# Kernel optimization log

Hardware: AMD Instinct MI355X
Metric: run time of the kernel (lower is better)

## Reference

```python
import jax, jax.numpy as jnp
import numpy as np

B, S, D, H = 2, 2048, 1024, 16
HD = D // H  # head_size = 64

def setup_inputs() -> dict:
    key = jax.random.key(0)
    ks = jax.random.split(key, 8)
    sc = 0.02
    return {
        "q": jax.random.normal(ks[0], (B, S, D), jnp.float32),
        "k": jax.random.normal(ks[1], (B, S, D), jnp.float32),
        "v": jax.random.normal(ks[2], (B, S, D), jnp.float32),
        "padding_mask": jnp.zeros((B, 1, 1, S), jnp.float32),
        "Wq": jax.random.normal(ks[3], (D, D), jnp.float32) * sc,
        "bq": jnp.zeros((D,), jnp.float32),
        "Wk": jax.random.normal(ks[4], (D, D), jnp.float32) * sc,
        "bk": jnp.zeros((D,), jnp.float32),
        "Wv": jax.random.normal(ks[5], (D, D), jnp.float32) * sc,
        "bv": jnp.zeros((D,), jnp.float32),
        "Wo": jax.random.normal(ks[6], (D, D), jnp.float32) * sc,
        "bo": jnp.zeros((D,), jnp.float32),
    }

def reference(q, k, v, padding_mask, Wq, bq, Wk, bk, Wv, bv, Wo, bo):
    b = q.shape[0]
    qh = (q @ Wq + bq).reshape(b, -1, H, HD)
    kh = (k @ Wk + bk).reshape(b, -1, H, HD)
    vh = (v @ Wv + bv).reshape(b, -1, H, HD)
    # [B, H, Sq, Sk] scores, materialized as in the original
    qk = jnp.einsum('bjhd,bkhd->bhjk', qh, kh) / jnp.sqrt(jnp.float32(HD))
    qk = qk + padding_mask * -1e12
    attn = jax.nn.softmax(qk, axis=-1)
    qkv = jnp.einsum('bhjk,bkhd->bjhd', attn, vh).reshape(b, -1, D)
    return qkv @ Wo + bo
```

## Files before the change

### kernel.cpp

```cpp
#include <hip/hip_runtime.h>
#include <math.h>

typedef __bf16 bf16_t;
typedef __bf16 bf16x8 __attribute__((ext_vector_type(8)));
typedef __bf16 bf16x4v __attribute__((ext_vector_type(4)));
typedef float f32x4 __attribute__((ext_vector_type(4)));
typedef float f32x16 __attribute__((ext_vector_type(16)));

#define LOG2E 1.4426950408889634f
#define MBIAS_C (-1e12f * LOG2E)

#if __has_builtin(__builtin_amdgcn_exp2f)
#define EXP2F(x) __builtin_amdgcn_exp2f(x)
#else
#define EXP2F(x) exp2f(x)
#endif

typedef __attribute__((address_space(1))) const unsigned int g_u32;
typedef __attribute__((address_space(3))) unsigned int l_u32;
__device__ __forceinline__ void load_lds_16B(const void* g, void* l){
  __builtin_amdgcn_global_load_lds((g_u32*)g, (l_u32*)l, 16, 0, 0);
}

__device__ __forceinline__ f32x16 zero16(){
  f32x16 z;
  #pragma unroll
  for (int i = 0; i < 16; i++) z[i] = 0.f;
  return z;
}

typedef union { bf16x4v b4; uint2 u2; } pk8;
typedef union { uint2 h[2]; bf16x8 b8; } pk16;
typedef union { float4 f4[4]; f32x16 v; } cinit_t;

__global__ __launch_bounds__(256) void cast3_kernel(const float* __restrict__ q,
                                                    const float* __restrict__ k,
                                                    const float* __restrict__ v,
                                                    bf16_t* __restrict__ out){
  int z = blockIdx.y;
  const float* x = (z == 0) ? q : (z == 1) ? k : v;
  int i = blockIdx.x * 256 + threadIdx.x;
  float4 f = reinterpret_cast<const float4*>(x)[i];
  bf16x4v w;
  w[0] = (bf16_t)f.x; w[1] = (bf16_t)f.y; w[2] = (bf16_t)f.z; w[3] = (bf16_t)f.w;
  reinterpret_cast<bf16x4v*>(out + (size_t)z * 4194304)[i] = w;
}

__global__ __launch_bounds__(256) void wtrans4_kernel(const float* __restrict__ Wq,
                                                      const float* __restrict__ Wk,
                                                      const float* __restrict__ Wv,
                                                      const float* __restrict__ Wo,
                                                      bf16_t* __restrict__ Wcat,
                                                      bf16_t* __restrict__ Wot){
  __shared__ float T[32][33];
  int z = blockIdx.z;
  const float* W = (z == 0) ? Wq : (z == 1) ? Wk : (z == 2) ? Wv : Wo;
  bf16_t* dst = (z < 3) ? (Wcat + (size_t)z * 1024 * 1024) : Wot;
  int x = threadIdx.x, y = threadIdx.y;
  int k0 = blockIdx.y * 32, n0 = blockIdx.x * 32;
  #pragma unroll
  for (int i = 0; i < 4; i++) T[y + 8*i][x] = W[(size_t)(k0 + y + 8*i) * 1024 + n0 + x];
  __syncthreads();
  #pragma unroll
  for (int i = 0; i < 4; i++) dst[(size_t)(n0 + y + 8*i) * 1024 + k0 + x] = (bf16_t)T[x][y + 8*i];
}

__device__ __forceinline__ void qkv_epilogue(f32x4 (&acc)[4][4], int seg, int n0g, int m0,
                                             int wm, int wn, int l16, int lq,
                                             const float* bias, bf16_t* qp, bf16_t* kp,
                                             bf16_t* vh){
  bf16_t* Cp = (seg == 0) ? qp : (seg == 1) ? kp : vh;
  float scale = (seg == 0) ? 0.125f * LOG2E : 1.0f;
  #pragma unroll
  for (int ti = 0; ti < 4; ti++){
    #pragma unroll
    for (int tj = 0; tj < 4; tj++){
      int col = (n0g + wn + tj*16 + l16) & 1023;
      float bvv = bias[col];
      #pragma unroll
      for (int r = 0; r < 4; r++){
        int row = m0 + wm + ti*16 + lq*4 + r;
        Cp[(size_t)row * 1024 + col] = (bf16_t)((acc[ti][tj][r] + bvv) * scale);
      }
    }
  }
}

__global__ __launch_bounds__(256) void gemm_qkv_bf(const bf16_t* __restrict__ qkvin,
                                                   const bf16_t* __restrict__ Wcat,
                                                   const float* __restrict__ bq,
                                                   const float* __restrict__ bk,
                                                   const float* __restrict__ bv,
                                                   bf16_t* __restrict__ qp,
                                                   bf16_t* __restrict__ kp,
                                                   bf16_t* __restrict__ vh){
  const int K = 1024;
  __shared__ __align__(16) bf16_t As[128*64];
  __shared__ __align__(16) bf16_t Bs[128*64];
  int tid = threadIdx.x, wave = tid >> 6, lane = tid & 63;
  int l16 = lane & 15, lq = lane >> 4;
  int m0  = blockIdx.x * 128;
  int n0g = blockIdx.y * 128;
  int seg = n0g >> 10;
  const bf16_t* A   = qkvin + (size_t)seg * 4194304;
  const float* bias = (seg == 0) ? bq : (seg == 1) ? bk : bv;
  int wm = (wave >> 1) * 64, wn = (wave & 1) * 64;
  f32x4 acc[4][4] = {};
  for (int kt = 0; kt < K; kt += 64){
    __syncthreads();
    #pragma unroll
    for (int i = 0; i < 4; i++){
      int u = tid + 256*i;
      int r = u >> 3, cpos = u & 7, cg = cpos ^ (r & 7);
      int ldsoff = (wave*64 + 256*i) * 16;
      load_lds_16B(&A[(size_t)(m0 + r) * K + kt + cg*8], (char*)As + ldsoff);
      load_lds_16B(&Wcat[(size_t)(n0g + r) * K + kt + cg*8], (char*)Bs + ldsoff);
    }
    __syncthreads();
    #pragma unroll
    for (int kk = 0; kk < 2; kk++){
      bf16x8 af[4], bfr[4];
      #pragma unroll
      for (int t = 0; t < 4; t++){
        int row = wm + t*16 + l16, cpos = (kk*4 + lq) ^ (l16 & 7);
        af[t] = *reinterpret_cast<bf16x8*>(&As[row*64 + cpos*8]);
      }
      #pragma unroll
      for (int t = 0; t < 4; t++){
        int row = wn + t*16 + l16, cpos = (kk*4 + lq) ^ (l16 & 7);
        bfr[t] = *reinterpret_cast<bf16x8*>(&Bs[row*64 + cpos*8]);
      }
      #pragma unroll
      for (int ti = 0; ti < 4; ti++)
        #pragma unroll
        for (int tj = 0; tj < 4; tj++)
          acc[ti][tj] = __builtin_amdgcn_mfma_f32_16x16x32_bf16(af[ti], bfr[tj], acc[ti][tj], 0, 0, 0);
    }
  }
  qkv_epilogue(acc, seg, n0g, m0, wm, wn, l16, lq, bias, qp, kp, vh);
}

__global__ __launch_bounds__(256) void gemm_qkv_f32(const float* __restrict__ qi,
                                                    const float* __restrict__ ki,
                                                    const float* __restrict__ vi,
                                                    const bf16_t* __restrict__ Wcat,
                                                    const float* __restrict__ bq,
                                                    const float* __restrict__ bk,
                                                    const float* __restrict__ bv,
                                                    bf16_t* __restrict__ qp,
                                                    bf16_t* __restrict__ kp,
                                                    bf16_t* __restrict__ vh){
  const int K = 1024;
  __shared__ __align__(16) float  Asf[128*32];
  __shared__ __align__(16) bf16_t Bs[128*32];
  int tid = threadIdx.x, wave = tid >> 6, lane = tid & 63;
  int l16 = lane & 15, lq = lane >> 4;
  int n0g = blockIdx.x * 128;
  int seg = n0g >> 10;
  const float* A    = (seg == 0) ? qi : (seg == 1) ? ki : vi;
  const float* bias = (seg == 0) ? bq : (seg == 1) ? bk : bv;
  int m0 = blockIdx.y * 128;
  int wm = (wave >> 1) * 64, wn = (wave & 1) * 64;
  int cposR = lq ^ ((l16 >> 2) & 3);
  int ca0 = (2*lq)     ^ (l16 & 7);
  int ca1 = (2*lq + 1) ^ (l16 & 7);
  f32x4 acc[4][4] = {};
  for (int kt = 0; kt < K; kt += 32){
    __syncthreads();
    #pragma unroll
    for (int i = 0; i < 4; i++){
      int u = tid + 256*i;
      int r = u >> 3, cpos = u & 7, cg = cpos ^ (r & 7);
      load_lds_16B(&A[(size_t)(m0 + r) * K + kt + cg*4], (char*)Asf + (wave*64 + 256*i)*16);
    }
    #pragma unroll
    for (int i = 0; i < 2; i++){
      int u = tid + 256*i;
      int r = u >> 2, cpos = u & 3, cg = cpos ^ ((r >> 2) & 3);
      load_lds_16B(&Wcat[(size_t)(n0g + r) * K + kt + cg*8], (char*)Bs + (wave*64 + 256*i)*16);
    }
    __syncthreads();
    bf16x8 af[4], bfr[4];
    #pragma unroll
    for (int t = 0; t < 4; t++){
      int row = wm + t*16 + l16;
      f32x4 x0 = *reinterpret_cast<f32x4*>(&Asf[row*32 + ca0*4]);
      f32x4 x1 = *reinterpret_cast<f32x4*>(&Asf[row*32 + ca1*4]);
      bf16x8 a;
      a[0] = (bf16_t)x0[0]; a[1] = (bf16_t)x0[1]; a[2] = (bf16_t)x0[2]; a[3] = (bf16_t)x0[3];
      a[4] = (bf16_t)x1[0]; a[5] = (bf16_t)x1[1]; a[6] = (bf16_t)x1[2]; a[7] = (bf16_t)x1[3];
      af[t] = a;
    }
    #pragma unroll
    for (int t = 0; t < 4; t++) bfr[t] = *reinterpret_cast<bf16x8*>(&Bs[(wn + t*16 + l16)*32 + cposR*8]);
    #pragma unroll
    for (int ti = 0; ti < 4; ti++)
      #pragma unroll
      for (int tj = 0; tj < 4; tj++)
        acc[ti][tj] = __builtin_amdgcn_mfma_f32_16x16x32_bf16(af[ti], bfr[tj], acc[ti][tj], 0, 0, 0);
  }
  qkv_epilogue(acc, seg, n0g, m0, wm, wn, l16, lq, bias, qp, kp, vh);
}

__global__ __launch_bounds__(256) void gemm_out(const bf16_t* __restrict__ A,
                                                const bf16_t* __restrict__ Bt,
                                                const float* __restrict__ bias,
                                                float* __restrict__ C){
  const int K = 1024, N = 1024;
  __shared__ __align__(16) bf16_t As[128*64];
  __shared__ __align__(16) bf16_t Bs[64*64];
  int tid = threadIdx.x, wave = tid >> 6, lane = tid & 63;
  int l16 = lane & 15, lq = lane >> 4;
  int m0 = blockIdx.x * 128, n0 = blockIdx.y * 64;
  int wm = wave * 32;
  f32x4 acc[2][4] = {};
  for (int kt = 0; kt < K; kt += 64){
    __syncthreads();
    #pragma unroll
    for (int i = 0; i < 4; i++){
      int u = tid + 256*i;
      int r = u >> 3, cpos = u & 7, cg = cpos ^ (r & 7);
      load_lds_16B(&A[(size_t)(m0 + r) * K + kt + cg*8], (char*)As + (wave*64 + 256*i)*16);
    }
    #pragma unroll
    for (int i = 0; i < 2; i++){
      int u = tid + 256*i;
      int r = u >> 3, cpos = u & 7, cg = cpos ^ (r & 7);
      load_lds_16B(&Bt[(size_t)(n0 + r) * K + kt + cg*8], (char*)Bs + (wave*64 + 256*i)*16);
    }
    __syncthreads();
    #pragma unroll
    for (int kk = 0; kk < 2; kk++){
      bf16x8 af[2], bfr[4];
      #pragma unroll
      for (int t = 0; t < 2; t++){
        int row = wm + t*16 + l16, cpos = (kk*4 + lq) ^ (l16 & 7);
        af[t] = *reinterpret_cast<bf16x8*>(&As[row*64 + cpos*8]);
      }
      #pragma unroll
      for (int t = 0; t < 4; t++){
        int row = t*16 + l16, cpos = (kk*4 + lq) ^ (l16 & 7);
        bfr[t] = *reinterpret_cast<bf16x8*>(&Bs[row*64 + cpos*8]);
      }
      #pragma unroll
      for (int ti = 0; ti < 2; ti++)
        #pragma unroll
        for (int tj = 0; tj < 4; tj++)
          acc[ti][tj] = __builtin_amdgcn_mfma_f32_16x16x32_bf16(af[ti], bfr[tj], acc[ti][tj], 0, 0, 0);
    }
  }
  #pragma unroll
  for (int ti = 0; ti < 2; ti++){
    #pragma unroll
    for (int tj = 0; tj < 4; tj++){
      int col = n0 + tj*16 + l16;
      float bvv = bias[col];
      #pragma unroll
      for (int r = 0; r < 4; r++){
        int row = m0 + wm + ti*16 + lq*4 + r;
        C[(size_t)row * N + col] = acc[ti][tj][r] + bvv;
      }
    }
  }
}

__global__ __launch_bounds__(256) void vtrans_kernel(const bf16_t* __restrict__ vh,
                                                     bf16_t* __restrict__ Vt){
  __shared__ bf16_t T[64][72];
  int tid = threadIdx.x;
  int s0 = blockIdx.x * 64, h = blockIdx.y, b = blockIdx.z;
  #pragma unroll
  for (int i = 0; i < 2; i++){
    int u = tid + 256*i;
    int r = u >> 3, c = (u & 7) * 8;
    *reinterpret_cast<uint4*>(&T[r][c]) =
      *reinterpret_cast<const uint4*>(&vh[(size_t)(b*2048 + s0 + r) * 1024 + h*64 + c]);
  }
  __syncthreads();
  #pragma unroll
  for (int i = 0; i < 2; i++){
    int u = tid + 256*i;
    int d = u >> 3, cs = (u & 7) * 8;
    bf16_t t8[8];
    #pragma unroll
    for (int j = 0; j < 8; j++) t8[j] = T[cs + j][d];
    *reinterpret_cast<uint4*>(&Vt[(size_t)((b*16 + h)*64 + d) * 2048 + s0 + cs]) =
      *reinterpret_cast<uint4*>(t8);
  }
}

__global__ __launch_bounds__(512, 4) void attn_kernel(const bf16_t* __restrict__ qp,
                                                      const bf16_t* __restrict__ kp,
                                                      const bf16_t* __restrict__ vt,
                                                      const float* __restrict__ mask,
                                                      bf16_t* __restrict__ ctx){
  const int S = 2048, D = 1024, HD = 64;
  __shared__ __align__(16) char smem[74240];
  float* Lsum  = (float*)(smem + 73728);
  float* Opart = (float*)smem;
  float* Mlw   = (float*)(smem + 65536);
  const float* Ml = Mlw;
  int tid = threadIdx.x, wave = tid >> 6, lane = tid & 63;
  int l32 = lane & 31, H = lane >> 5;
  int qo = wave >> 1, khalf = wave & 1;
  int h = blockIdx.x, b = blockIdx.y, qt = blockIdx.z;
  const bf16_t* Qg = qp + (size_t)b*S*D + h*HD;
  const bf16_t* Kg = kp + (size_t)b*S*D + h*HD;
  const bf16_t* Vg = vt + (size_t)(b*16 + h)*HD*S;
  const float*  Mg = mask + (size_t)b*S;

  auto stage = [&](int kt, int bsel){
    char* Kd = smem + bsel*8192;
    char* Vd = smem + 32768 + bsel*8192;
    int r = tid >> 3, c = tid & 7, cg = c ^ (r & 7);
    int ldsoff = wave * 1024;
    load_lds_16B(&Kg[(size_t)(kt + r) * D + cg*8], Kd + ldsoff);
    load_lds_16B(&Vg[(size_t)r * S + kt + cg*8], Vd + ldsoff);
  };

  int qrow = qt*128 + qo*32 + l32;
  bf16x8 qf[4];
  #pragma unroll
  for (int s = 0; s < 4; s++)
    qf[s] = *reinterpret_cast<const bf16x8*>(&Qg[(size_t)qrow * D + s*16 + 8*H]);

  f32x16 o0 = zero16(), o1 = zero16(), lmm = zero16();
  int krow = khalf*32 + l32;

  pk16 ones;
  ones.h[0].x = 0x3F803F80u; ones.h[0].y = 0x3F803F80u;
  ones.h[1].x = 0x3F803F80u; ones.h[1].y = 0x3F803F80u;

  load_lds_16B(&Mg[(size_t)tid*4], smem + 65536 + wave*1024);
  stage(0, 0);
  stage(64, 1);
  __syncthreads();
  {
    f32x4 mv = *reinterpret_cast<f32x4*>(&Mlw[tid*4]);
    mv *= MBIAS_C;
    *reinterpret_cast<f32x4*>(&Mlw[tid*4]) = mv;
  }
  __syncthreads();

  auto tile_compute = [&](int kt, int cur){
    bf16_t* Ks  = (bf16_t*)(smem + cur*8192);
    bf16_t* Vts = (bf16_t*)(smem + 32768 + cur*8192);
    cinit_t ci;
    #pragma unroll
    for (int g = 0; g < 4; g++)
      ci.f4[g] = *reinterpret_cast<const float4*>(&Ml[kt + khalf*32 + 8*g + 4*H]);
    f32x16 sc;
    __builtin_amdgcn_s_setprio(1);
    #pragma unroll
    for (int s = 0; s < 4; s++){
      int cp = (2*s + H) ^ (l32 & 7);
      bf16x8 kf = *reinterpret_cast<bf16x8*>(&Ks[krow*64 + cp*8]);
      if (s == 0) sc = __builtin_amdgcn_mfma_f32_32x32x16_bf16(kf, qf[0], ci.v, 0, 0, 0);
      else        sc = __builtin_amdgcn_mfma_f32_32x32x16_bf16(kf, qf[s], sc, 0, 0, 0);
    }
    __builtin_amdgcn_s_setprio(0);
    pk8 grp[4];
    #pragma unroll
    for (int g = 0; g < 4; g++){
      float p0 = EXP2F(sc[4*g+0]);
      float p1 = EXP2F(sc[4*g+1]);
      float p2 = EXP2F(sc[4*g+2]);
      float p3 = EXP2F(sc[4*g+3]);
      pk8 w;
      w.b4[0] = (bf16_t)p0; w.b4[1] = (bf16_t)p1; w.b4[2] = (bf16_t)p2; w.b4[3] = (bf16_t)p3;
      grp[g] = w;
    }
    #pragma unroll
    for (int kk = 0; kk < 2; kk++){
      uint2 ga = grp[2*kk].u2;
      uint2 gb = grp[2*kk+1].u2;
      uint2 send = H ? ga : gb;
      uint2 recv;
      recv.x = (unsigned)__shfl_xor((int)send.x, 32);
      recv.y = (unsigned)__shfl_xor((int)send.y, 32);
      pk16 fr;
      fr.h[0] = H ? recv : ga;
      fr.h[1] = H ? gb : recv;
      int cp = (4*khalf + 2*kk + H) ^ (l32 & 7);
      bf16x8 vf0 = *reinterpret_cast<bf16x8*>(&Vts[l32*64 + cp*8]);
      bf16x8 vf1 = *reinterpret_cast<bf16x8*>(&Vts[(32 + l32)*64 + cp*8]);
      __builtin_amdgcn_s_setprio(1);
      o0  = __builtin_amdgcn_mfma_f32_32x32x16_bf16(fr.b8, vf0, o0, 0, 0, 0);
      o1  = __builtin_amdgcn_mfma_f32_32x32x16_bf16(fr.b8, vf1, o1, 0, 0, 0);
      lmm = __builtin_amdgcn_mfma_f32_32x32x16_bf16(fr.b8, ones.b8, lmm, 0, 0, 0);
      __builtin_amdgcn_s_setprio(0);
    }
  };

  #pragma unroll 2
  for (int it = 0; it < 16; ++it){
    int kt = it * 128;
    if (it < 15){
      stage(kt + 128, (2*it + 2) & 3);
      stage(kt + 192, (2*it + 3) & 3);
    }
    tile_compute(kt,      (2*it) & 3);
    tile_compute(kt + 64, (2*it + 1) & 3);
    __syncthreads();
  }

  if (khalf == 1){
    #pragma unroll
    for (int reg = 0; reg < 16; reg++){
      Opart[qo*2048 + reg*64 + lane]        = o0[reg];
      Opart[qo*2048 + 1024 + reg*64 + lane] = o1[reg];
    }
    if (l32 == 0){
      #pragma unroll
      for (int reg = 0; reg < 16; reg++)
        Lsum[qo*32 + (reg & 3) + 8*(reg >> 2) + 4*H] = lmm[reg];
    }
  }
  __syncthreads();
  if (khalf == 0){
    #pragma unroll
    for (int reg = 0; reg < 16; reg++){
      o0[reg] += Opart[qo*2048 + reg*64 + lane];
      o1[reg] += Opart[qo*2048 + 1024 + reg*64 + lane];
    }
    #pragma unroll
    for (int g = 0; g < 4; g++){
      #pragma unroll
      for (int r = 0; r < 4; r++){
        float lf = lmm[4*g + r] + Lsum[qo*32 + 8*g + 4*H + r];
        float inv = 1.f / lf;
        int grow = qt*128 + qo*32 + 8*g + 4*H + r;
        size_t base = (size_t)(b*S + grow) * D + h*HD;
        ctx[base + l32]      = (bf16_t)(o0[4*g + r] * inv);
        ctx[base + 32 + l32] = (bf16_t)(o1[4*g + r] * inv);
      }
    }
  }
}

extern "C" void kernel_launch(void* const* d_in, const int* in_sizes, int n_in,
                              void* d_out, int out_size, void* d_ws, size_t ws_size,
                              hipStream_t stream){
  const float* q    = (const float*)d_in[0];
  const float* k    = (const float*)d_in[1];
  const float* v    = (const float*)d_in[2];
  const float* mask = (const float*)d_in[3];
  const float* Wq   = (const float*)d_in[4];
  const float* bq   = (const float*)d_in[5];
  const float* Wk   = (const float*)d_in[6];
  const float* bk   = (const float*)d_in[7];
  const float* Wv   = (const float*)d_in[8];
  const float* bv   = (const float*)d_in[9];
  const float* Wo   = (const float*)d_in[10];
  const float* bo   = (const float*)d_in[11];

  char* ws = (char*)d_ws;
  bf16_t* qp    = (bf16_t*)(ws);
  bf16_t* kp    = (bf16_t*)(ws + 8388608);
  bf16_t* vh    = (bf16_t*)(ws + 16777216);
  bf16_t* Wcat  = (bf16_t*)(ws + 25165824);
  bf16_t* Wot   = (bf16_t*)(ws + 31457280);
  bf16_t* Vt    = (bf16_t*)(ws + 33554432);
  bf16_t* ctx   = (bf16_t*)(ws + 41943040);
  bf16_t* qkvin = (bf16_t*)(ws + 33554432);

  wtrans4_kernel<<<dim3(32,32,4), dim3(32,8), 0, stream>>>(Wq, Wk, Wv, Wo, Wcat, Wot);
  if (ws_size >= 58720256){
    cast3_kernel<<<dim3(4096,3), 256, 0, stream>>>(q, k, v, qkvin);
    gemm_qkv_bf<<<dim3(32,24), 256, 0, stream>>>(qkvin, Wcat, bq, bk, bv, qp, kp, vh);
  } else {
    gemm_qkv_f32<<<dim3(24,32), 256, 0, stream>>>(q, k, v, Wcat, bq, bk, bv, qp, kp, vh);
  }
  vtrans_kernel<<<dim3(32,16,2), 256, 0, stream>>>(vh, Vt);
  attn_kernel<<<dim3(16,2,16), 512, 0, stream>>>(qp, kp, Vt, mask, ctx);
  gemm_out<<<dim3(32,16), 256, 0, stream>>>(ctx, Wot, bo, (float*)d_out);
}
```

Baseline: 231.8 us.

## Fuse cast and weight-transpose launches, double-buffer LDS in QKV and output GEMMs

```diff
diff --git a/kernel.cpp b/kernel.cpp
--- a/kernel.cpp
+++ b/kernel.cpp
@@ -33,36 +33,40 @@
 typedef union { uint2 h[2]; bf16x8 b8; } pk16;
 typedef union { float4 f4[4]; f32x16 v; } cinit_t;
 
-__global__ __launch_bounds__(256) void cast3_kernel(const float* __restrict__ q,
-                                                    const float* __restrict__ k,
-                                                    const float* __restrict__ v,
-                                                    bf16_t* __restrict__ out){
-  int z = blockIdx.y;
-  const float* x = (z == 0) ? q : (z == 1) ? k : v;
-  int i = blockIdx.x * 256 + threadIdx.x;
-  float4 f = reinterpret_cast<const float4*>(x)[i];
-  bf16x4v w;
-  w[0] = (bf16_t)f.x; w[1] = (bf16_t)f.y; w[2] = (bf16_t)f.z; w[3] = (bf16_t)f.w;
-  reinterpret_cast<bf16x4v*>(out + (size_t)z * 4194304)[i] = w;
-}
-
-__global__ __launch_bounds__(256) void wtrans4_kernel(const float* __restrict__ Wq,
-                                                      const float* __restrict__ Wk,
-                                                      const float* __restrict__ Wv,
-                                                      const float* __restrict__ Wo,
-                                                      bf16_t* __restrict__ Wcat,
-                                                      bf16_t* __restrict__ Wot){
+__global__ __launch_bounds__(256) void prep_kernel(const float* __restrict__ q,
+                                                   const float* __restrict__ k,
+                                                   const float* __restrict__ v,
+                                                   const float* __restrict__ Wq,
+                                                   const float* __restrict__ Wk,
+                                                   const float* __restrict__ Wv,
+                                                   const float* __restrict__ Wo,
+                                                   bf16_t* __restrict__ qkvin,
+                                                   bf16_t* __restrict__ Wcat,
+                                                   bf16_t* __restrict__ Wot,
+                                                   int cast_blocks){
   __shared__ float T[32][33];
-  int z = blockIdx.z;
-  const float* W = (z == 0) ? Wq : (z == 1) ? Wk : (z == 2) ? Wv : Wo;
-  bf16_t* dst = (z < 3) ? (Wcat + (size_t)z * 1024 * 1024) : Wot;
-  int x = threadIdx.x, y = threadIdx.y;
-  int k0 = blockIdx.y * 32, n0 = blockIdx.x * 32;
-  #pragma unroll
-  for (int i = 0; i < 4; i++) T[y + 8*i][x] = W[(size_t)(k0 + y + 8*i) * 1024 + n0 + x];
-  __syncthreads();
-  #pragma unroll
-  for (int i = 0; i < 4; i++) dst[(size_t)(n0 + y + 8*i) * 1024 + k0 + x] = (bf16_t)T[x][y + 8*i];
+  int id = blockIdx.x, tid = threadIdx.x;
+  if (id < cast_blocks){
+    int z = id >> 12;
+    int i = (id & 4095) * 256 + tid;
+    const float* x = (z == 0) ? q : (z == 1) ? k : v;
+    float4 f = reinterpret_cast<const float4*>(x)[i];
+    bf16x4v w;
+    w[0] = (bf16_t)f.x; w[1] = (bf16_t)f.y; w[2] = (bf16_t)f.z; w[3] = (bf16_t)f.w;
+    reinterpret_cast<bf16x4v*>(qkvin + (size_t)z * 4194304)[i] = w;
+  } else {
+    int wid = id - cast_blocks;
+    int z = wid >> 10, t = wid & 1023;
+    int k0 = (t >> 5) * 32, n0 = (t & 31) * 32;
+    int x = tid & 31, y = tid >> 5;
+    const float* W = (z == 0) ? Wq : (z == 1) ? Wk : (z == 2) ? Wv : Wo;
+    bf16_t* dst = (z < 3) ? (Wcat + (size_t)z * 1024 * 1024) : Wot;
+    #pragma unroll
+    for (int i = 0; i < 4; i++) T[y + 8*i][x] = W[(size_t)(k0 + y + 8*i) * 1024 + n0 + x];
+    __syncthreads();
+    #pragma unroll
+    for (int i = 0; i < 4; i++) dst[(size_t)(n0 + y + 8*i) * 1024 + k0 + x] = (bf16_t)T[x][y + 8*i];
+  }
 }
 
 __device__ __forceinline__ void qkv_epilogue(f32x4 (&acc)[4][4], int seg, int n0g, int m0,
@@ -95,8 +99,8 @@
                                                    bf16_t* __restrict__ kp,
                                                    bf16_t* __restrict__ vh){
   const int K = 1024;
-  __shared__ __align__(16) bf16_t As[128*64];
-  __shared__ __align__(16) bf16_t Bs[128*64];
+  __shared__ __align__(16) bf16_t As[2][128*32];
+  __shared__ __align__(16) bf16_t Bs[2][128*32];
   int tid = threadIdx.x, wave = tid >> 6, lane = tid & 63;
   int l16 = lane & 15, lq = lane >> 4;
   int m0  = blockIdx.x * 128;
@@ -105,37 +109,39 @@
   const bf16_t* A   = qkvin + (size_t)seg * 4194304;
   const float* bias = (seg == 0) ? bq : (seg == 1) ? bk : bv;
   int wm = (wave >> 1) * 64, wn = (wave & 1) * 64;
+  int cposR = lq ^ ((l16 >> 2) & 3);
   f32x4 acc[4][4] = {};
-  for (int kt = 0; kt < K; kt += 64){
-    __syncthreads();
-    #pragma unroll
-    for (int i = 0; i < 4; i++){
+
+  auto stage = [&](int kt, int bsel){
+    #pragma unroll
+    for (int i = 0; i < 2; i++){
       int u = tid + 256*i;
-      int r = u >> 3, cpos = u & 7, cg = cpos ^ (r & 7);
+      int r = u >> 2, cpos = u & 3, cg = cpos ^ ((r >> 2) & 3);
       int ldsoff = (wave*64 + 256*i) * 16;
-      load_lds_16B(&A[(size_t)(m0 + r) * K + kt + cg*8], (char*)As + ldsoff);
-      load_lds_16B(&Wcat[(size_t)(n0g + r) * K + kt + cg*8], (char*)Bs + ldsoff);
-    }
-    __syncthreads();
-    #pragma unroll
-    for (int kk = 0; kk < 2; kk++){
-      bf16x8 af[4], bfr[4];
-      #pragma unroll
-      for (int t = 0; t < 4; t++){
-        int row = wm + t*16 + l16, cpos = (kk*4 + lq) ^ (l16 & 7);
-        af[t] = *reinterpret_cast<bf16x8*>(&As[row*64 + cpos*8]);
-      }
-      #pragma unroll
-      for (int t = 0; t < 4; t++){
-        int row = wn + t*16 + l16, cpos = (kk*4 + lq) ^ (l16 & 7);
-        bfr[t] = *reinterpret_cast<bf16x8*>(&Bs[row*64 + cpos*8]);
-      }
-      #pragma unroll
-      for (int ti = 0; ti < 4; ti++)
-        #pragma unroll
-        for (int tj = 0; tj < 4; tj++)
-          acc[ti][tj] = __builtin_amdgcn_mfma_f32_16x16x32_bf16(af[ti], bfr[tj], acc[ti][tj], 0, 0, 0);
-    }
+      load_lds_16B(&A[(size_t)(m0 + r) * K + kt + cg*8], (char*)As[bsel] + ldsoff);
+      load_lds_16B(&Wcat[(size_t)(n0g + r) * K + kt + cg*8], (char*)Bs[bsel] + ldsoff);
+    }
+  };
+  auto compute = [&](int cur){
+    bf16x8 af[4], bfr[4];
+    #pragma unroll
+    for (int t = 0; t < 4; t++) af[t]  = *reinterpret_cast<bf16x8*>(&As[cur][(wm + t*16 + l16)*32 + cposR*8]);
+    #pragma unroll
+    for (int t = 0; t < 4; t++) bfr[t] = *reinterpret_cast<bf16x8*>(&Bs[cur][(wn + t*16 + l16)*32 + cposR*8]);
+    #pragma unroll
+    for (int ti = 0; ti < 4; ti++)
+      #pragma unroll
+      for (int tj = 0; tj < 4; tj++)
+        acc[ti][tj] = __builtin_amdgcn_mfma_f32_16x16x32_bf16(af[ti], bfr[tj], acc[ti][tj], 0, 0, 0);
+  };
+
+  stage(0, 0);
+  __syncthreads();
+  #pragma unroll 1
+  for (int it = 0; it < 32; ++it){
+    if (it < 31) stage((it + 1) * 32, (it + 1) & 1);
+    compute(it & 1);
+    __syncthreads();
   }
   qkv_epilogue(acc, seg, n0g, m0, wm, wn, l16, lq, bias, qp, kp, vh);
 }
@@ -207,40 +213,41 @@
                                                 const float* __restrict__ bias,
                                                 float* __restrict__ C){
   const int K = 1024, N = 1024;
-  __shared__ __align__(16) bf16_t As[128*64];
-  __shared__ __align__(16) bf16_t Bs[64*64];
+  __shared__ __align__(16) bf16_t As[2][128*64];
+  __shared__ __align__(16) bf16_t Bs[2][64*64];
   int tid = threadIdx.x, wave = tid >> 6, lane = tid & 63;
   int l16 = lane & 15, lq = lane >> 4;
   int m0 = blockIdx.x * 128, n0 = blockIdx.y * 64;
   int wm = wave * 32;
   f32x4 acc[2][4] = {};
-  for (int kt = 0; kt < K; kt += 64){
-    __syncthreads();
+
+  auto stage = [&](int kt, int bsel){
     #pragma unroll
     for (int i = 0; i < 4; i++){
       int u = tid + 256*i;
       int r = u >> 3, cpos = u & 7, cg = cpos ^ (r & 7);
-      load_lds_16B(&A[(size_t)(m0 + r) * K + kt + cg*8], (char*)As + (wave*64 + 256*i)*16);
+      load_lds_16B(&A[(size_t)(m0 + r) * K + kt + cg*8], (char*)As[bsel] + (wave*64 + 256*i)*16);
     }
     #pragma unroll
     for (int i = 0; i < 2; i++){
       int u = tid + 256*i;
       int r = u >> 3, cpos = u & 7, cg = cpos ^ (r & 7);
-      load_lds_16B(&Bt[(size_t)(n0 + r) * K + kt + cg*8], (char*)Bs + (wave*64 + 256*i)*16);
-    }
-    __syncthreads();
+      load_lds_16B(&Bt[(size_t)(n0 + r) * K + kt + cg*8], (char*)Bs[bsel] + (wave*64 + 256*i)*16);
+    }
+  };
+  auto compute = [&](int cur){
     #pragma unroll
     for (int kk = 0; kk < 2; kk++){
       bf16x8 af[2], bfr[4];
       #pragma unroll
       for (int t = 0; t < 2; t++){
         int row = wm + t*16 + l16, cpos = (kk*4 + lq) ^ (l16 & 7);
-        af[t] = *reinterpret_cast<bf16x8*>(&As[row*64 + cpos*8]);
+        af[t] = *reinterpret_cast<bf16x8*>(&As[cur][row*64 + cpos*8]);
       }
       #pragma unroll
       for (int t = 0; t < 4; t++){
         int row = t*16 + l16, cpos = (kk*4 + lq) ^ (l16 & 7);
-        bfr[t] = *reinterpret_cast<bf16x8*>(&Bs[row*64 + cpos*8]);
+        bfr[t] = *reinterpret_cast<bf16x8*>(&Bs[cur][row*64 + cpos*8]);
       }
       #pragma unroll
       for (int ti = 0; ti < 2; ti++)
@@ -248,7 +255,17 @@
         for (int tj = 0; tj < 4; tj++)
           acc[ti][tj] = __builtin_amdgcn_mfma_f32_16x16x32_bf16(af[ti], bfr[tj], acc[ti][tj], 0, 0, 0);
     }
-  }
+  };
+
+  stage(0, 0);
+  __syncthreads();
+  #pragma unroll 1
+  for (int it = 0; it < 16; ++it){
+    if (it < 15) stage((it + 1) * 64, (it + 1) & 1);
+    compute(it & 1);
+    __syncthreads();
+  }
+
   #pragma unroll
   for (int ti = 0; ti < 2; ti++){
     #pragma unroll
@@ -464,11 +481,11 @@
   bf16_t* ctx   = (bf16_t*)(ws + 41943040);
   bf16_t* qkvin = (bf16_t*)(ws + 33554432);
 
-  wtrans4_kernel<<<dim3(32,32,4), dim3(32,8), 0, stream>>>(Wq, Wk, Wv, Wo, Wcat, Wot);
   if (ws_size >= 58720256){
-    cast3_kernel<<<dim3(4096,3), 256, 0, stream>>>(q, k, v, qkvin);
+    prep_kernel<<<dim3(16384), 256, 0, stream>>>(q, k, v, Wq, Wk, Wv, Wo, qkvin, Wcat, Wot, 12288);
     gemm_qkv_bf<<<dim3(32,24), 256, 0, stream>>>(qkvin, Wcat, bq, bk, bv, qp, kp, vh);
   } else {
+    prep_kernel<<<dim3(4096), 256, 0, stream>>>(q, k, v, Wq, Wk, Wv, Wo, qkvin, Wcat, Wot, 0);
     gemm_qkv_f32<<<dim3(24,32), 256, 0, stream>>>(q, k, v, Wcat, bq, bk, bv, qp, kp, vh);
   }
   vtrans_kernel<<<dim3(32,16,2), 256, 0, stream>>>(vh, Vt);
```

After: 224.6 us. -3.1%, faster.
